# Optimization experiments

Hardware: AMD Instinct MI355X
Metric: run time of the kernel (lower is better)

## Reference

```python
import jax, jax.numpy as jnp
import numpy as np

N = 8192       # n_concepts
D = 128        # embed_dim
L = 2          # n_layers
ALPHA = 0.7
BETA = 0.3
LAM = 0.1      # lambda_decay


def setup_inputs() -> dict:
    key = jax.random.key(0)
    ks = jax.random.split(key, 16)
    adj = jax.random.randint(ks[0], (N, N), 0, 2).astype(jnp.float32)
    s = 0.05
    return {
        "adj": adj,
        "concept_embed": jax.random.normal(ks[1], (N, D), jnp.float32) * s,
        # torch Linear weight is [out,in]; stored here as [in,out] for x @ W
        "gc_w": jax.random.normal(ks[2], (L, D, D), jnp.float32) * s,
        "gc_b": jnp.zeros((L, D), jnp.float32),
        "wq": jax.random.normal(ks[3], (D, D), jnp.float32) * s,
        "bq": jnp.zeros((D,), jnp.float32),
        "wk": jax.random.normal(ks[4], (D, D), jnp.float32) * s,
        "bk": jnp.zeros((D,), jnp.float32),
        "wv": jax.random.normal(ks[5], (D, D), jnp.float32) * s,
        "bv": jnp.zeros((D,), jnp.float32),
        "g1_w": jax.random.normal(ks[6], (4 * D, 2 * D), jnp.float32) * s,
        "g1_b": jnp.zeros((2 * D,), jnp.float32),
        "g2_w": jax.random.normal(ks[7], (2 * D, 4), jnp.float32) * s,
        "g2_b": jnp.zeros((4,), jnp.float32),
        "layer_weights": jnp.ones((L,), jnp.float32) / L,
    }


def _aggregate(E, adj, wq, bq, wk, bk, wv, bv, g1_w, g1_b, g2_w, g2_b):
    nbr = adj != 0                                            # [N,N] neighbor pattern
    nrm = jnp.maximum(jnp.linalg.norm(E, axis=1), 1e-8)       # torch cosine_similarity eps
    sim = (E @ E.T) / (nrm[:, None] * nrm[None, :])           # [N,N] cosine sims
    pos = nbr & (sim >= ALPHA)
    neg = nbr & (sim <= BETA)
    bnd = nbr & (sim > BETA) & (sim < ALPHA)
    posf = pos.astype(E.dtype)
    negf = neg.astype(E.dtype)
    # masked means (zero when region empty, matching torch zeros fallback)
    pos_emb = (posf @ E) / jnp.maximum(posf.sum(1, keepdims=True), 1.0)
    neg_emb = LAM * (negf @ E) / jnp.maximum(negf.sum(1, keepdims=True), 1.0)
    # boundary region: attention of node i over its boundary neighbors
    Q = E @ wq + bq
    K = E @ wk + bk
    V = E @ wv + bv
    s = (Q @ K.T) / np.sqrt(D).astype(np.float32)             # [N,N]
    m = jnp.max(jnp.where(bnd, s, -jnp.inf), axis=1, keepdims=True)
    m = jnp.where(jnp.isfinite(m), m, 0.0)                    # safe max when region empty
    e = jnp.where(bnd, jnp.exp(s - m), 0.0)
    w = e / jnp.maximum(e.sum(1, keepdims=True), 1e-30)       # masked softmax (0 if empty)
    bnd_emb = w @ V
    # gated fusion of [self, pos, bound, neg]
    concat = jnp.concatenate([E, pos_emb, bnd_emb, neg_emb], axis=1)  # [N,4D]
    h = jax.nn.relu(concat @ g1_w + g1_b)
    gate = jax.nn.softmax(h @ g2_w + g2_b, axis=-1)           # [N,4]
    regions = jnp.stack([E, pos_emb, bnd_emb, neg_emb], axis=1)  # [N,4,D]
    fused = jnp.einsum('nr,nrd->nd', gate, regions)
    # nodes with no neighbors keep their own embedding
    return jnp.where(nbr.any(axis=1, keepdims=True), fused, E)


def reference(adj, concept_embed, gc_w, gc_b, wq, bq, wk, bk, wv, bv,
              g1_w, g1_b, g2_w, g2_b, layer_weights):
    cur = concept_embed
    outs = []
    for l in range(L):
        agg = _aggregate(cur, adj, wq, bq, wk, bk, wv, bv, g1_w, g1_b, g2_w, g2_b)
        cur = jax.nn.relu(agg @ gc_w[l] + gc_b[l])
        outs.append(cur)
    lw = jax.nn.softmax(layer_weights)
    return jnp.einsum('l,lnd->nd', lw, jnp.stack(outs))
```

## Files before the change

### kernel.cpp

```cpp
#include <hip/hip_runtime.h>
#include <stdint.h>

#define NN 8192
#define DD 128
#define ALPHA 0.7f
#define BETA 0.3f
#define LAM 0.1f
#define QSCALE 0.08838834764831845f
#define DELTA 3e-5f
#define DELTA_L1 9e-3f
#define FLAGCAP 262144
#define FLAG2CAP 1048576

typedef __attribute__((ext_vector_type(8))) short short8;
typedef __attribute__((ext_vector_type(4))) float f32x4;
typedef unsigned short ush;

__device__ __forceinline__ ush f2bf(float f){
  union { float f; unsigned u; } v; v.f = f;
  return (ush)((v.u + 0x7FFFu + ((v.u >> 16) & 1u)) >> 16);
}
__device__ __forceinline__ float bf2f(ush s){
  union { unsigned u; float f; } v; v.u = ((unsigned)s) << 16; return v.f;
}

__device__ __forceinline__ float qkdot(const ush* __restrict__ Qh,
                                       const ush* __restrict__ Kh,
                                       int i, int j, int lane){
  float q0 = bf2f(Qh[i*DD + lane]),      k0 = bf2f(Kh[j*DD + lane]);
  float q1 = bf2f(Qh[i*DD + 64 + lane]), k1 = bf2f(Kh[j*DD + 64 + lane]);
  float s = q0*k0 + q1*k1;
  #pragma unroll
  for (int m = 32; m; m >>= 1) s += __shfl_xor(s, m, 64);
  return s;
}

__global__ void k_init(const float* __restrict__ adj, unsigned* __restrict__ adjw,
                       const float* __restrict__ wq, const float* __restrict__ wk,
                       const float* __restrict__ wv, const float* __restrict__ g1w,
                       const float* __restrict__ gcw,
                       ush* __restrict__ qkvTh, ush* __restrict__ qkvTl,
                       ush* __restrict__ g1wTh, ush* __restrict__ g1wTl,
                       ush* __restrict__ gcwTh, ush* __restrict__ gcwTl){
  if (blockIdx.x < NN){
    int i = blockIdx.x, wave = threadIdx.x >> 6, lane = threadIdx.x & 63;
    for (int seg = wave; seg < 128; seg += 4){
      int j = seg*64 + lane;
      unsigned long long bm = __ballot(adj[(size_t)i*NN + j] != 0.0f);
      if (lane == 0)  adjw[i*256 + seg*2]     = (unsigned)bm;
      if (lane == 32) adjw[i*256 + seg*2 + 1] = (unsigned)(bm >> 32);
    }
    return;
  }
  int idx = (blockIdx.x - NN)*256 + threadIdx.x;
  const float* src; ush *dh, *dl; int K, Nout, li;
  if      (idx <  16384){ src=wq;        dh=qkvTh;        dl=qkvTl;        K=128; Nout=128; li=idx; }
  else if (idx <  32768){ src=wk;        dh=qkvTh+16384;  dl=qkvTl+16384;  K=128; Nout=128; li=idx-16384; }
  else if (idx <  49152){ src=wv;        dh=qkvTh+32768;  dl=qkvTl+32768;  K=128; Nout=128; li=idx-32768; }
  else if (idx < 180224){ src=g1w;       dh=g1wTh;        dl=g1wTl;        K=512; Nout=256; li=idx-49152; }
  else if (idx < 196608){ src=gcw;       dh=gcwTh;        dl=gcwTl;        K=128; Nout=128; li=idx-180224; }
  else if (idx < 212992){ src=gcw+16384; dh=gcwTh+16384;  dl=gcwTl+16384;  K=128; Nout=128; li=idx-196608; }
  else return;
  int k = li / Nout, n = li - k*Nout;
  float v = src[li];
  ush h = f2bf(v);
  dh[n*K + k] = h;
  dl[n*K + k] = f2bf(v - bf2f(h));
}

__global__ void k_prep(const float* __restrict__ E, double* __restrict__ nrm64,
                       ush* __restrict__ Enh, ush* __restrict__ Enl,
                       ush* __restrict__ EhiT, ush* __restrict__ EloT,
                       const ush* __restrict__ BtH, const ush* __restrict__ BtL,
                       const float* __restrict__ bq, const float* __restrict__ bk,
                       const float* __restrict__ bv,
                       ush* __restrict__ Qh, ush* __restrict__ Kh,
                       ush* __restrict__ VhT, ush* __restrict__ VloT){
  __shared__ float t[64][65];
  __shared__ float sV[128*33];
  int bid = blockIdx.x, tid = threadIdx.x;
  if (bid < 2048){
    int i = bid*4 + (tid >> 6);
    int l = tid & 63;
    float v0 = E[i*DD + l], v1 = E[i*DD + 64 + l];
    double ss = (double)v0*(double)v0 + (double)v1*(double)v1;
    #pragma unroll
    for (int m = 32; m; m >>= 1) ss += __shfl_xor(ss, m, 64);
    double nr = sqrt(ss); if (nr < 1e-8) nr = 1e-8;
    float inv = (float)(1.0 / nr);
    float n0 = v0*inv, n1 = v1*inv;
    ush h0 = f2bf(n0), h1 = f2bf(n1);
    Enh[i*DD + l] = h0;       Enh[i*DD + 64 + l] = h1;
    Enl[i*DD + l] = f2bf(n0 - bf2f(h0));
    Enl[i*DD + 64 + l] = f2bf(n1 - bf2f(h1));
    if (l == 0) nrm64[i] = nr;
  } else if (bid < 2304){
    int lin = bid - 2048;
    int r0 = (lin >> 1) * 64, c0 = (lin & 1) * 64;
    for (int idx = tid; idx < 4096; idx += 256){
      int r = idx >> 6, c = idx & 63;
      t[r][c] = E[(r0 + r)*DD + c0 + c];
    }
    __syncthreads();
    for (int idx = tid; idx < 4096; idx += 256){
      int c = idx >> 6, r = idx & 63;
      float v = t[r][c];
      ush h = f2bf(v);
      EhiT[(size_t)(c0 + c)*NN + r0 + r] = h;
      EloT[(size_t)(c0 + c)*NN + r0 + r] = f2bf(v - bf2f(h));
    }
  } else {
    int lane = tid & 63, wave = tid >> 6;
    int l15 = lane & 15, quad = lane >> 4;
    int rowblk = (bid - 2304) * 32;
    int row16 = rowblk + (wave >> 1)*16;
    int nf0 = (wave & 1)*12;
    f32x4 acc[12];
    #pragma unroll
    for (int i = 0; i < 12; i++){ f32x4 z = {0.f,0.f,0.f,0.f}; acc[i] = z; }
    #pragma unroll
    for (int kk = 0; kk < 4; kk++){
      const float* ap = &E[(row16 + l15)*DD + kk*32 + quad*8];
      short8 ah, al;
      #pragma unroll
      for (int j = 0; j < 8; j++){
        float v = ap[j];
        ush h = f2bf(v);
        ah[j] = (short)h; al[j] = (short)f2bf(v - bf2f(h));
      }
      #pragma unroll
      for (int i = 0; i < 12; i++){
        int bo = ((nf0 + i)*16 + l15)*DD + kk*32 + quad*8;
        short8 bh = *(const short8*)&BtH[bo];
        short8 bl = *(const short8*)&BtL[bo];
        acc[i] = __builtin_amdgcn_mfma_f32_16x16x32_bf16(ah, bh, acc[i], 0, 0, 0);
        acc[i] = __builtin_amdgcn_mfma_f32_16x16x32_bf16(al, bh, acc[i], 0, 0, 0);
        acc[i] = __builtin_amdgcn_mfma_f32_16x16x32_bf16(ah, bl, acc[i], 0, 0, 0);
      }
    }
    #pragma unroll
    for (int i = 0; i < 12; i++){
      int nfg = nf0 + i;
      int grp = nfg >> 3;
      int col = (nfg & 7)*16 + l15;
      float b = (grp == 0) ? bq[col] : (grp == 1) ? bk[col] : bv[col];
      #pragma unroll
      for (int r = 0; r < 4; r++){
        int row = row16 + quad*4 + r;
        float v = acc[i][r] + b;
        if (grp == 0)      Qh[row*DD + col] = f2bf(v * QSCALE);
        else if (grp == 1) Kh[row*DD + col] = f2bf(v);
        else               sV[col*33 + (row - rowblk)] = v;
      }
    }
    __syncthreads();
    int feat = tid >> 1, rh = (tid & 1)*16;
    ush hh[16], ll[16];
    #pragma unroll
    for (int j = 0; j < 16; j++){
      float v = sV[feat*33 + rh + j];
      ush h = f2bf(v);
      hh[j] = h; ll[j] = f2bf(v - bf2f(h));
    }
    size_t go = (size_t)feat*NN + rowblk + rh;
    *(uint4*)&VhT [go]     = *(const uint4*)&hh[0];
    *(uint4*)&VhT [go + 8] = *(const uint4*)&hh[8];
    *(uint4*)&VloT[go]     = *(const uint4*)&ll[0];
    *(uint4*)&VloT[go + 8] = *(const uint4*)&ll[8];
  }
}

__global__ void k_mlp(const float* __restrict__ E, const float* __restrict__ P,
                      const float* __restrict__ B, const float* __restrict__ N,
                      const float* __restrict__ cntP, const float* __restrict__ cntN,
                      const float* __restrict__ denB,
                      const ush* __restrict__ g1Th, const ush* __restrict__ g1Tl,
                      const float* __restrict__ g1b,
                      const float* __restrict__ g2w, const float* __restrict__ g2b,
                      const ush* __restrict__ gcTh, const ush* __restrict__ gcTl,
                      const float* __restrict__ gcb,
                      const float* __restrict__ prevC, const float* __restrict__ lwv,
                      int dofinal, float* __restrict__ out){
  __shared__ float sH[16*260];
  int tid = threadIdx.x, lane = tid & 63, wave = tid >> 6;
  int l15 = lane & 15, quad = lane >> 4;
  int row16 = blockIdx.x*16;
  int row = row16 + l15;
  float cp = cntP[row], cn = cntN[row], dn = denB[row];
  {
    int nf0 = wave*4;
    float rs[4] = {1.f, 1.f/fmaxf(cp,1.f), (dn > 0.5f) ? (1.f/dn) : 0.f, LAM/fmaxf(cn,1.f)};
    const float* bases[4] = {E, P, B, N};
    f32x4 acc[4];
    #pragma unroll
    for (int nf = 0; nf < 4; nf++){ f32x4 z = {0.f,0.f,0.f,0.f}; acc[nf] = z; }
    #pragma unroll
    for (int kk = 0; kk < 16; kk++){
      const float* ap = &bases[kk>>2][row*DD + (kk&3)*32 + quad*8];
      float sc = rs[kk>>2];
      short8 ah, al;
      #pragma unroll
      for (int j = 0; j < 8; j++){
        float v = ap[j] * sc;
        ush h = f2bf(v);
        ah[j] = (short)h; al[j] = (short)f2bf(v - bf2f(h));
      }
      #pragma unroll
      for (int nf = 0; nf < 4; nf++){
        int bo = ((nf0 + nf)*16 + l15)*512 + kk*32 + quad*8;
        short8 bh = *(const short8*)&g1Th[bo];
        short8 bl = *(const short8*)&g1Tl[bo];
        acc[nf] = __builtin_amdgcn_mfma_f32_16x16x32_bf16(ah, bh, acc[nf], 0, 0, 0);
        acc[nf] = __builtin_amdgcn_mfma_f32_16x16x32_bf16(al, bh, acc[nf], 0, 0, 0);
        acc[nf] = __builtin_amdgcn_mfma_f32_16x16x32_bf16(ah, bl, acc[nf], 0, 0, 0);
      }
    }
    #pragma unroll
    for (int nf = 0; nf < 4; nf++){
      int col = (nf0 + nf)*16 + l15;
      float b = g1b[col];
      #pragma unroll
      for (int r = 0; r < 4; r++)
        sH[(quad*4 + r)*260 + col] = fmaxf(acc[nf][r] + b, 0.f);
    }
  }
  __syncthreads();
  {
    int nf0 = wave*2;
    float l0=0,l1=0,l2=0,l3=0;
    #pragma unroll
    for (int i = 0; i < 16; i++){
      float4 hv = *(const float4*)&sH[l15*260 + quad*64 + i*4];
      float hvv[4] = {hv.x, hv.y, hv.z, hv.w};
      #pragma unroll
      for (int j = 0; j < 4; j++){
        float4 w4 = *(const float4*)&g2w[(quad*64 + i*4 + j)*4];
        l0 = fmaf(hvv[j], w4.x, l0); l1 = fmaf(hvv[j], w4.y, l1);
        l2 = fmaf(hvv[j], w4.z, l2); l3 = fmaf(hvv[j], w4.w, l3);
      }
    }
    l0 += __shfl_xor(l0,16,64); l0 += __shfl_xor(l0,32,64);
    l1 += __shfl_xor(l1,16,64); l1 += __shfl_xor(l1,32,64);
    l2 += __shfl_xor(l2,16,64); l2 += __shfl_xor(l2,32,64);
    l3 += __shfl_xor(l3,16,64); l3 += __shfl_xor(l3,32,64);
    l0 += g2b[0]; l1 += g2b[1]; l2 += g2b[2]; l3 += g2b[3];
    float mx = fmaxf(fmaxf(l0,l1), fmaxf(l2,l3));
    float e0 = __expf(l0-mx), e1 = __expf(l1-mx), e2 = __expf(l2-mx), e3 = __expf(l3-mx);
    float inv = 1.f/(e0+e1+e2+e3);
    float g0 = e0*inv, g1v = e1*inv, g2v = e2*inv, g3 = e3*inv;
    bool any = (cp + cn > 0.5f) || (dn > 0.5f);
    float pscl = g1v/fmaxf(cp,1.f);
    float bscl = (dn > 0.5f) ? (g2v/dn) : 0.f;
    float nscl = LAM*g3/fmaxf(cn,1.f);
    f32x4 acc[2];
    #pragma unroll
    for (int nf = 0; nf < 2; nf++){ f32x4 z = {0.f,0.f,0.f,0.f}; acc[nf] = z; }
    #pragma unroll
    for (int kk = 0; kk < 4; kk++){
      int koff = row*DD + kk*32 + quad*8;
      short8 ah, al;
      #pragma unroll
      for (int j = 0; j < 8; j++){
        float ev = E[koff + j];
        float v = any ? (g0*ev + pscl*P[koff+j] + bscl*B[koff+j] + nscl*N[koff+j]) : ev;
        ush h = f2bf(v);
        ah[j] = (short)h; al[j] = (short)f2bf(v - bf2f(h));
      }
      #pragma unroll
      for (int nf = 0; nf < 2; nf++){
        int bo = ((nf0 + nf)*16 + l15)*DD + kk*32 + quad*8;
        short8 bh = *(const short8*)&gcTh[bo];
        short8 bl = *(const short8*)&gcTl[bo];
        acc[nf] = __builtin_amdgcn_mfma_f32_16x16x32_bf16(ah, bh, acc[nf], 0, 0, 0);
        acc[nf] = __builtin_amdgcn_mfma_f32_16x16x32_bf16(al, bh, acc[nf], 0, 0, 0);
        acc[nf] = __builtin_amdgcn_mfma_f32_16x16x32_bf16(ah, bl, acc[nf], 0, 0, 0);
      }
    }
    float we0 = 0.5f, we1 = 0.5f;
    if (dofinal){
      float a0 = lwv[0], a1 = lwv[1];
      float mw = fmaxf(a0, a1);
      float x0 = __expf(a0-mw), x1 = __expf(a1-mw);
      float iv = 1.f/(x0+x1);
      we0 = x0*iv; we1 = x1*iv;
    }
    #pragma unroll
    for (int nf = 0; nf < 2; nf++){
      int col = (nf0 + nf)*16 + l15;
      float b = gcb[col];
      #pragma unroll
      for (int r = 0; r < 4; r++){
        int rr = row16 + quad*4 + r;
        float val = fmaxf(acc[nf][r] + b, 0.f);
        if (dofinal) val = we0*prevC[rr*DD + col] + we1*val;
        out[rr*DD + col] = val;
      }
    }
  }
}

#define BM 64
#define BN 32
#define CSPLIT 4
#define CCHUNK (NN/CSPLIT)
#define NTILES (CCHUNK/BN)
#define RSTRIDE 136
#define FSTRIDE 80
#define MSTRIDE 80

template<int DENSEB>
__launch_bounds__(256, 2)
__global__ void k_fused(const unsigned* __restrict__ adjw,
    const ush* __restrict__ Enh, const ush* __restrict__ Enl,
    const ush* __restrict__ Qh,  const ush* __restrict__ Kh,
    const ush* __restrict__ EhiT, const ush* __restrict__ EloT,
    const ush* __restrict__ VhT,  const ush* __restrict__ VloT,
    float* __restrict__ Nsum, float* __restrict__ Bsum,
    float* __restrict__ cntN, float* __restrict__ denB,
    int* __restrict__ flagCnt, float4* __restrict__ flags,
    int* __restrict__ flag2Cnt, float4* __restrict__ flags2)
{
  __shared__ __attribute__((aligned(16))) ush sEnh[32*RSTRIDE];
  __shared__ __attribute__((aligned(16))) ush sEnl[DENSEB ? 32*RSTRIDE : 16];
  __shared__ __attribute__((aligned(16))) ush sKh [DENSEB ? 32*RSTRIDE : 16];
  __shared__ __attribute__((aligned(16))) ush sE2 [128*FSTRIDE];
  __shared__ __attribute__((aligned(16))) ush sV2 [DENSEB ? 128*FSTRIDE : 16];
  __shared__ __attribute__((aligned(16))) ush sM  [4][16*MSTRIDE];

  const float del = DENSEB ? DELTA : DELTA_L1;
  int tid = threadIdx.x, lane = tid & 63, wave = tid >> 6;
  int l15 = lane & 15, quad = lane >> 4;
  int rowblk = blockIdx.x >> 2, split = blockIdx.x & 3;
  int row0 = rowblk * BM + wave * 16;
  int col0 = split * CCHUNK;

  short8 bEnh[4], bEnl[4], bQ[4];
  #pragma unroll
  for (int kf = 0; kf < 4; kf++){
    int go = (row0 + l15)*DD + kf*32 + quad*8;
    bEnh[kf] = *(const short8*)&Enh[go];
    if (DENSEB){
      bEnl[kf] = *(const short8*)&Enl[go];
      bQ[kf] = *(const short8*)&Qh[go];
    }
  }

  f32x4 accN[8], accB[DENSEB ? 8 : 1];
  #pragma unroll
  for (int nf = 0; nf < 8; nf++){ f32x4 z = {0.f,0.f,0.f,0.f}; accN[nf]=z; }
  if (DENSEB){
    #pragma unroll
    for (int nf = 0; nf < 8; nf++){ f32x4 z = {0.f,0.f,0.f,0.f}; accB[nf]=z; }
  }
  float cnL = 0.f, dbL = 0.f;

  int f0 = tid >> 2,        n0 = (tid & 3)*8;
  int f1 = (tid+256) >> 2,  n1 = ((tid+256) & 3)*8;
  uint4 pEh0, pEh1, pVh0, pVh1;
  {
    size_t g0 = (size_t)f0*NN + col0 + n0, g1 = (size_t)f1*NN + col0 + n1;
    pEh0 = *(const uint4*)&EhiT[g0]; pEh1 = *(const uint4*)&EhiT[g1];
    if (DENSEB){
      pVh0 = *(const uint4*)&VhT [g0]; pVh1 = *(const uint4*)&VhT [g1];
    }
  }
  int rr0 = tid >> 4,       ro0 = (tid & 15)*8;
  int rr1 = (tid+256) >> 4, ro1 = ((tid+256) & 15)*8;

  for (int t = 0; t < NTILES; t++){
    int c0 = col0 + t*BN;
    __syncthreads();
    *(uint4*)&sE2[f0*FSTRIDE + n0] = pEh0;  *(uint4*)&sE2[f1*FSTRIDE + n1] = pEh1;
    if (DENSEB){
      *(uint4*)&sV2[f0*FSTRIDE + n0] = pVh0;  *(uint4*)&sV2[f1*FSTRIDE + n1] = pVh1;
    }
    {
      uint4 a0 = *(const uint4*)&Enh[(c0 + rr0)*DD + ro0];
      uint4 a1 = *(const uint4*)&Enh[(c0 + rr1)*DD + ro1];
      *(uint4*)&sEnh[rr0*RSTRIDE + ro0] = a0;  *(uint4*)&sEnh[rr1*RSTRIDE + ro1] = a1;
      if (DENSEB){
        uint4 b0 = *(const uint4*)&Enl[(c0 + rr0)*DD + ro0];
        uint4 b1 = *(const uint4*)&Enl[(c0 + rr1)*DD + ro1];
        uint4 k0 = *(const uint4*)&Kh [(c0 + rr0)*DD + ro0];
        uint4 k1 = *(const uint4*)&Kh [(c0 + rr1)*DD + ro1];
        *(uint4*)&sEnl[rr0*RSTRIDE + ro0] = b0;  *(uint4*)&sEnl[rr1*RSTRIDE + ro1] = b1;
        *(uint4*)&sKh [rr0*RSTRIDE + ro0] = k0;  *(uint4*)&sKh [rr1*RSTRIDE + ro1] = k1;
      }
    }
    __syncthreads();
    if (t + 1 < NTILES){
      int c1 = c0 + BN;
      size_t g0 = (size_t)f0*NN + c1 + n0, g1 = (size_t)f1*NN + c1 + n1;
      pEh0 = *(const uint4*)&EhiT[g0]; pEh1 = *(const uint4*)&EhiT[g1];
      if (DENSEB){
        pVh0 = *(const uint4*)&VhT [g0]; pVh1 = *(const uint4*)&VhT [g1];
      }
    }
    unsigned aw = adjw[(row0 + l15)*256 + (c0 >> 5)];

    f32x4 simT[2], svT[2];
    { f32x4 z = {0.f,0.f,0.f,0.f}; simT[0]=z; simT[1]=z; svT[0]=z; svT[1]=z; }
    #pragma unroll
    for (int f = 0; f < 2; f++){
      #pragma unroll
      for (int kf = 0; kf < 4; kf++){
        int la = (f*16 + l15)*RSTRIDE + kf*32 + quad*8;
        short8 ch = *(const short8*)&sEnh[la];
        simT[f] = __builtin_amdgcn_mfma_f32_16x16x32_bf16(ch, bEnh[kf], simT[f],0,0,0);
        if (DENSEB){
          short8 cl = *(const short8*)&sEnl[la];
          short8 ck = *(const short8*)&sKh [la];
          simT[f] = __builtin_amdgcn_mfma_f32_16x16x32_bf16(cl, bEnh[kf], simT[f],0,0,0);
          simT[f] = __builtin_amdgcn_mfma_f32_16x16x32_bf16(ch, bEnl[kf], simT[f],0,0,0);
          svT [f] = __builtin_amdgcn_mfma_f32_16x16x32_bf16(ck, bQ  [kf], svT [f],0,0,0);
        }
      }
    }
    ushort4 ehv[2];
    unsigned flagb = 0, spb = 0;
    #pragma unroll
    for (int f = 0; f < 2; f++){
      ush vn2[4], veh[4];
      #pragma unroll
      for (int r = 0; r < 4; r++){
        int cbit = f*16 + quad*4 + r;
        bool nbr = (aw >> cbit) & 1u;
        float c = simT[f][r];
        bool pos = nbr && (c >= ALPHA);
        bool neg = nbr && (c <= BETA);
        bool bnd = nbr && !pos && !neg;
        vn2[r] = neg ? (ush)0x3F80 : (ush)0;
        cnL += neg ? 1.f : 0.f;
        if (DENSEB){
          float e = bnd ? __expf(svT[f][r]) : 0.f;
          veh[r] = f2bf(e);
          dbL += e;
        }
        if (nbr && (fabsf(c - ALPHA) < del || fabsf(c - BETA) < del))
          flagb |= 1u << (f*4 + r);
        if (pos || (!DENSEB && bnd))
          spb |= 1u << (f*4 + r);
      }
      int mb = l15*MSTRIDE + f*16 + quad*4;
      *(ushort4*)&sM[wave][mb] = make_ushort4(vn2[0],vn2[1],vn2[2],vn2[3]);
      if (DENSEB)
        ehv[f] = make_ushort4(veh[0],veh[1],veh[2],veh[3]);
    }
    if (__ballot((flagb | spb) != 0)){
      #pragma unroll
      for (int f = 0; f < 2; f++){
        #pragma unroll
        for (int r = 0; r < 4; r++){
          int bit = f*4 + r;
          bool fl = (flagb >> bit) & 1u;
          unsigned long long bm = __ballot(fl);
          if (bm){
            int leader = __ffsll((long long)bm) - 1;
            int base = 0;
            if (lane == leader) base = atomicAdd(flagCnt, __popcll(bm));
            base = __shfl(base, leader, 64);
            if (fl){
              int id = base + __popcll(bm & ((1ull << lane) - 1ull));
              if (id < FLAGCAP){
                float4 rec;
                rec.x = __int_as_float(row0 + l15);
                rec.y = __int_as_float(c0 + f*16 + quad*4 + r);
                rec.z = simT[f][r];
                rec.w = DENSEB ? svT[f][r] : 0.f;
                flags[id] = rec;
              }
            }
          }
          bool f2 = (spb >> bit) & 1u;
          unsigned long long bm2 = __ballot(f2);
          if (bm2){
            int leader = __ffsll((long long)bm2) - 1;
            int base = 0;
            if (lane == leader) base = atomicAdd(flag2Cnt, __popcll(bm2));
            base = __shfl(base, leader, 64);
            if (f2){
              int id = base + __popcll(bm2 & ((1ull << lane) - 1ull));
              if (id < FLAG2CAP){
                float c = simT[f][r];
                int j = c0 + f*16 + quad*4 + r;
                int cls = (c >= ALPHA) ? 0 : 1;
                float4 rec;
                rec.x = __int_as_float(row0 + l15);
                rec.y = __int_as_float(j | (cls << 16));
                rec.z = c;
                rec.w = DENSEB ? svT[f][r] : 0.f;
                flags2[id] = rec;
              }
            }
          }
        }
      }
    }
    {
      short8 mNeg = *(const short8*)&sM[wave][l15*MSTRIDE + quad*8];
      #pragma unroll
      for (int nf = 0; nf < 8; nf++){
        int so = (nf*16 + l15)*FSTRIDE + quad*8;
        short8 eth = *(const short8*)&sE2[so];
        accN[nf] = __builtin_amdgcn_mfma_f32_16x16x32_bf16(mNeg, eth, accN[nf],0,0,0);
      }
    }
    if (DENSEB){
      int mb0 = l15*MSTRIDE + quad*4;
      *(ushort4*)&sM[wave][mb0]      = ehv[0];
      *(ushort4*)&sM[wave][mb0 + 16] = ehv[1];
      short8 mEh = *(const short8*)&sM[wave][l15*MSTRIDE + quad*8];
      #pragma unroll
      for (int nf = 0; nf < 8; nf++){
        int so = (nf*16 + l15)*FSTRIDE + quad*8;
        short8 vth = *(const short8*)&sV2[so];
        accB[nf] = __builtin_amdgcn_mfma_f32_16x16x32_bf16(mEh, vth, accB[nf],0,0,0);
      }
    }
  }
  #pragma unroll
  for (int nf = 0; nf < 8; nf++){
    int col = nf*16 + l15;
    #pragma unroll
    for (int r = 0; r < 4; r++){
      int row = row0 + quad*4 + r;
      atomicAdd(&Nsum[row*DD + col], accN[nf][r]);
      if (DENSEB) atomicAdd(&Bsum[row*DD + col], accB[nf][r]);
    }
  }
  cnL += __shfl_xor(cnL, 16, 64); cnL += __shfl_xor(cnL, 32, 64);
  if (DENSEB){ dbL += __shfl_xor(dbL, 16, 64); dbL += __shfl_xor(dbL, 32, 64); }
  if (quad == 0){
    atomicAdd(&cntN[row0 + l15], cnL);
    if (DENSEB) atomicAdd(&denB[row0 + l15], dbL);
  }
}

__global__ void k_fix(const float* __restrict__ E, const double* __restrict__ nrm64,
    const ush* __restrict__ EhiT, const ush* __restrict__ EloT,
    const ush* __restrict__ VhT,  const ush* __restrict__ VloT,
    const ush* __restrict__ Qh,   const ush* __restrict__ Kh, int dotmode,
    const int* __restrict__ flag2Cnt, const float4* __restrict__ flags2,
    const int* __restrict__ flagCnt,  const float4* __restrict__ flags,
    float* __restrict__ Psum, float* __restrict__ Nsum, float* __restrict__ Bsum,
    float* __restrict__ cntP, float* __restrict__ cntN, float* __restrict__ denB)
{
  int lane = threadIdx.x & 63;
  if (blockIdx.x < 256){
    int cnt = *flag2Cnt; if (cnt > FLAG2CAP) cnt = FLAG2CAP;
    int gw = (blockIdx.x * blockDim.x + threadIdx.x) >> 6;
    int nw = (256 * blockDim.x) >> 6;
    for (int idx = gw; idx < cnt; idx += nw){
      float4 rec = flags2[idx];
      int i = __float_as_int(rec.x);
      int jraw = __float_as_int(rec.y);
      int j = jraw & 0xFFFF, cls = jraw >> 16;
      if (cls == 0){
        #pragma unroll
        for (int h = 0; h < 2; h++){
          int d = lane + h*64;
          float ev = bf2f(EhiT[(size_t)d*NN + j]) + bf2f(EloT[(size_t)d*NN + j]);
          atomicAdd(&Psum[i*DD + d], ev);
        }
        if (lane == 0) atomicAdd(&cntP[i], 1.f);
      } else {
        float s = dotmode ? qkdot(Qh, Kh, i, j, lane) : rec.w;
        float e = __expf(s);
        float ehf = bf2f(f2bf(e));
        float elf = bf2f(f2bf(e - ehf));
        #pragma unroll
        for (int h = 0; h < 2; h++){
          int d = lane + h*64;
          float vh = bf2f(VhT [(size_t)d*NN + j]);
          float bv = ehf*vh;
          if (dotmode) bv += elf*vh + ehf*bf2f(VloT[(size_t)d*NN + j]);
          atomicAdd(&Bsum[i*DD + d], bv);
        }
        if (lane == 0) atomicAdd(&denB[i], e);
      }
    }
  } else {
    int cnt = *flagCnt; if (cnt > FLAGCAP) cnt = FLAGCAP;
    int gw = ((blockIdx.x - 256) * blockDim.x + threadIdx.x) >> 6;
    int nw = (512 * blockDim.x) >> 6;
    for (int idx = gw; idx < cnt; idx += nw){
      float4 rec = flags[idx];
      int i = __float_as_int(rec.x), j = __float_as_int(rec.y);
      float c = rec.z;
      float ei0 = E[i*DD + lane], ei1 = E[i*DD + 64 + lane];
      float ej0 = E[j*DD + lane], ej1 = E[j*DD + 64 + lane];
      double d = (double)ei0*(double)ej0 + (double)ei1*(double)ej1;
      #pragma unroll
      for (int m = 32; m; m >>= 1) d += __shfl_xor(d, m, 64);
      double se = d / (nrm64[i]*nrm64[j]);
      int ce = (se >= (double)ALPHA) ? 0 : ((se <= (double)BETA) ? 1 : 2);
      int cc = (c >= ALPHA) ? 0 : ((c <= BETA) ? 1 : 2);
      if (ce == cc) continue;
      float s = dotmode ? qkdot(Qh, Kh, i, j, lane) : rec.w;
      float e = __expf(s);
      float ehf = bf2f(f2bf(e));
      float elf = bf2f(f2bf(e - ehf));
      #pragma unroll
      for (int h = 0; h < 2; h++){
        int dd2 = lane + h*64;
        float evh = bf2f(EhiT[(size_t)dd2*NN + j]);
        float evp = evh + bf2f(EloT[(size_t)dd2*NN + j]);
        float vh = bf2f(VhT[(size_t)dd2*NN + j]);
        float bv = ehf*vh;
        if (dotmode) bv += elf*vh + ehf*bf2f(VloT[(size_t)dd2*NN + j]);
        float subv = (cc==0) ? -evp : (cc==1) ? -evh : -bv;
        float* subA = (cc==0) ? Psum : (cc==1) ? Nsum : Bsum;
        atomicAdd(&subA[i*DD + dd2], subv);
        float addv = (ce==0) ? evp : (ce==1) ? evh : bv;
        float* addA = (ce==0) ? Psum : (ce==1) ? Nsum : Bsum;
        atomicAdd(&addA[i*DD + dd2], addv);
      }
      if (lane == 0){
        float* subC = (cc==0) ? cntP : (cc==1) ? cntN : denB;
        atomicAdd(&subC[i], (cc==2) ? -e : -1.f);
        float* addC = (ce==0) ? cntP : (ce==1) ? cntN : denB;
        atomicAdd(&addC[i], (ce==2) ?  e :  1.f);
      }
    }
  }
}

extern "C" void kernel_launch(void* const* d_in, const int* in_sizes, int n_in,
                              void* d_out, int out_size, void* d_ws, size_t ws_size,
                              hipStream_t stream){
  const float* adj   = (const float*)d_in[0];
  const float* embed = (const float*)d_in[1];
  const float* gc_w  = (const float*)d_in[2];
  const float* gc_b  = (const float*)d_in[3];
  const float* wq = (const float*)d_in[4];
  const float* bq = (const float*)d_in[5];
  const float* wk = (const float*)d_in[6];
  const float* bk = (const float*)d_in[7];
  const float* wv = (const float*)d_in[8];
  const float* bv = (const float*)d_in[9];
  const float* g1w = (const float*)d_in[10];
  const float* g1b = (const float*)d_in[11];
  const float* g2w = (const float*)d_in[12];
  const float* g2b = (const float*)d_in[13];
  const float* lw  = (const float*)d_in[14];
  float* out = (float*)d_out;

  char* p = (char*)d_ws;
  auto alloc = [&](size_t bytes)->void*{ void* r = (void*)p; p += (bytes + 255) & ~(size_t)255; return r; };
  ush* qkvTh = (ush*)alloc(384*128*2);  ush* qkvTl = (ush*)alloc(384*128*2);
  ush* g1wTh = (ush*)alloc(512*256*2);  ush* g1wTl = (ush*)alloc(512*256*2);
  ush* gcwTh = (ush*)alloc(2*128*128*2); ush* gcwTl = (ush*)alloc(2*128*128*2);
  unsigned* adjw = (unsigned*)alloc((size_t)NN*256*4);
  double* nrm64 = (double*)alloc(NN*8);
  ush* Enh  = (ush*)alloc((size_t)NN*DD*2);
  ush* Enl  = (ush*)alloc((size_t)NN*DD*2);
  ush* EhiT = (ush*)alloc((size_t)NN*DD*2);
  ush* EloT = (ush*)alloc((size_t)NN*DD*2);
  ush* Qh   = (ush*)alloc((size_t)NN*DD*2);
  ush* Khb  = (ush*)alloc((size_t)NN*DD*2);
  ush* VhT  = (ush*)alloc((size_t)NN*DD*2);
  ush* VloT = (ush*)alloc((size_t)NN*DD*2);
  char* zbase = p;
  float* Psum = (float*)alloc((size_t)NN*DD*4);
  float* Nsum = (float*)alloc((size_t)NN*DD*4);
  float* Bsum = (float*)alloc((size_t)NN*DD*4);
  float* cntP = (float*)alloc(NN*4);
  float* cntN = (float*)alloc(NN*4);
  float* denB = (float*)alloc(NN*4);
  int*   flagCnt  = (int*)alloc(256);
  int*   flag2Cnt = (int*)alloc(256);
  size_t zbytes = (size_t)(p - zbase);
  float4* flags  = (float4*)alloc((size_t)FLAGCAP*16);
  float4* flags2 = (float4*)alloc((size_t)FLAG2CAP*16);
  float* cur0 = (float*)alloc((size_t)NN*DD*4);

  k_init<<<NN + 832, 256, 0, stream>>>(adj, adjw, wq, wk, wv, g1w, gc_w,
      qkvTh, qkvTl, g1wTh, g1wTl, gcwTh, gcwTl);

  const float* Ecur = embed;
  for (int l = 0; l < 2; l++){
    k_prep<<<2560, 256, 0, stream>>>(Ecur, nrm64, Enh, Enl, EhiT, EloT,
        qkvTh, qkvTl, bq, bk, bv, Qh, Khb, VhT, VloT);
    hipMemsetAsync(zbase, 0, zbytes, stream);
    if (l == 0)
      k_fused<0><<<(NN/BM)*CSPLIT, 256, 0, stream>>>(adjw, Enh, Enl, Qh, Khb,
          EhiT, EloT, VhT, VloT, Nsum, Bsum, cntN, denB,
          flagCnt, flags, flag2Cnt, flags2);
    else
      k_fused<1><<<(NN/BM)*CSPLIT, 256, 0, stream>>>(adjw, Enh, Enl, Qh, Khb,
          EhiT, EloT, VhT, VloT, Nsum, Bsum, cntN, denB,
          flagCnt, flags, flag2Cnt, flags2);
    k_fix<<<768, 256, 0, stream>>>(Ecur, nrm64, EhiT, EloT, VhT, VloT,
        Qh, Khb, (l == 0) ? 1 : 0, flag2Cnt, flags2, flagCnt, flags,
        Psum, Nsum, Bsum, cntP, cntN, denB);
    k_mlp<<<512, 256, 0, stream>>>(Ecur, Psum, Bsum, Nsum, cntP, cntN, denB,
        g1wTh, g1wTl, g1b, g2w, g2b,
        gcwTh + l*128*128, gcwTl + l*128*128, gc_b + l*128,
        cur0, lw, l, (l == 0) ? cur0 : out);
    Ecur = (l == 0) ? cur0 : out;
  }
}
```

Baseline: 1.045 ms.

## Double column split in fused kernel and replace atomics with partial-sum reduction

Raises the column split from 4 to 8 so the fused kernel launches twice as many blocks. It shrinks the shared-memory strides to match the smaller chunk and raises occupancy hints to 3 blocks per CU. Per-split partial sums are written to separate buffers with plain stores instead of float atomics, and a new reduce kernel sums them before the fix stage. This trades atomic contention for roughly 64 MB of extra partial-buffer traffic and one more kernel launch per layer.

```diff
diff --git a/kernel.cpp b/kernel.cpp
--- a/kernel.cpp
+++ b/kernel.cpp
@@ -167,6 +167,44 @@
     *(uint4*)&VhT [go + 8] = *(const uint4*)&hh[8];
     *(uint4*)&VloT[go]     = *(const uint4*)&ll[0];
     *(uint4*)&VloT[go + 8] = *(const uint4*)&ll[8];
+  }
+}
+
+__global__ void k_reduce(const float4* __restrict__ NsumP, const float4* __restrict__ BsumP,
+                         const float* __restrict__ cntNP, const float* __restrict__ denBP,
+                         float4* __restrict__ Nsum, float4* __restrict__ Bsum,
+                         float* __restrict__ cntN, float* __restrict__ denB, int doB){
+  const int NE4 = NN*DD/4;
+  int idx = blockIdx.x*256 + threadIdx.x;
+  if (idx < NE4){
+    float4 a = NsumP[idx];
+    #pragma unroll
+    for (int s = 1; s < 8; s++){
+      float4 u = NsumP[(size_t)s*NE4 + idx];
+      a.x += u.x; a.y += u.y; a.z += u.z; a.w += u.w;
+    }
+    Nsum[idx] = a;
+    if (doB){
+      float4 b = BsumP[idx];
+      #pragma unroll
+      for (int s = 1; s < 8; s++){
+        float4 u = BsumP[(size_t)s*NE4 + idx];
+        b.x += u.x; b.y += u.y; b.z += u.z; b.w += u.w;
+      }
+      Bsum[idx] = b;
+    }
+  } else if (idx < NE4 + NN){
+    int r = idx - NE4;
+    float c = 0.f;
+    #pragma unroll
+    for (int s = 0; s < 8; s++) c += cntNP[s*NN + r];
+    cntN[r] = c;
+    if (doB){
+      float d2 = 0.f;
+      #pragma unroll
+      for (int s = 0; s < 8; s++) d2 += denBP[s*NN + r];
+      denB[r] = d2;
+    }
   }
 }
 
@@ -301,22 +339,22 @@
 
 #define BM 64
 #define BN 32
-#define CSPLIT 4
+#define CSPLIT 8
 #define CCHUNK (NN/CSPLIT)
 #define NTILES (CCHUNK/BN)
 #define RSTRIDE 136
-#define FSTRIDE 80
-#define MSTRIDE 80
+#define FSTRIDE 40
+#define MSTRIDE 40
 
 template<int DENSEB>
-__launch_bounds__(256, 2)
+__launch_bounds__(256, 3)
 __global__ void k_fused(const unsigned* __restrict__ adjw,
     const ush* __restrict__ Enh, const ush* __restrict__ Enl,
     const ush* __restrict__ Qh,  const ush* __restrict__ Kh,
     const ush* __restrict__ EhiT, const ush* __restrict__ EloT,
     const ush* __restrict__ VhT,  const ush* __restrict__ VloT,
-    float* __restrict__ Nsum, float* __restrict__ Bsum,
-    float* __restrict__ cntN, float* __restrict__ denB,
+    float* __restrict__ NsumP, float* __restrict__ BsumP,
+    float* __restrict__ cntNP, float* __restrict__ denBP,
     int* __restrict__ flagCnt, float4* __restrict__ flags,
     int* __restrict__ flag2Cnt, float4* __restrict__ flags2)
 {
@@ -330,7 +368,7 @@
   const float del = DENSEB ? DELTA : DELTA_L1;
   int tid = threadIdx.x, lane = tid & 63, wave = tid >> 6;
   int l15 = lane & 15, quad = lane >> 4;
-  int rowblk = blockIdx.x >> 2, split = blockIdx.x & 3;
+  int rowblk = blockIdx.x >> 3, split = blockIdx.x & 7;
   int row0 = rowblk * BM + wave * 16;
   int col0 = split * CCHUNK;
 
@@ -518,21 +556,23 @@
       }
     }
   }
+  float* Np = NsumP + (size_t)split*(NN*DD);
+  float* Bp = BsumP + (size_t)split*(NN*DD);
   #pragma unroll
   for (int nf = 0; nf < 8; nf++){
     int col = nf*16 + l15;
     #pragma unroll
     for (int r = 0; r < 4; r++){
       int row = row0 + quad*4 + r;
-      atomicAdd(&Nsum[row*DD + col], accN[nf][r]);
-      if (DENSEB) atomicAdd(&Bsum[row*DD + col], accB[nf][r]);
+      Np[row*DD + col] = accN[nf][r];
+      if (DENSEB) Bp[row*DD + col] = accB[nf][r];
     }
   }
   cnL += __shfl_xor(cnL, 16, 64); cnL += __shfl_xor(cnL, 32, 64);
   if (DENSEB){ dbL += __shfl_xor(dbL, 16, 64); dbL += __shfl_xor(dbL, 32, 64); }
   if (quad == 0){
-    atomicAdd(&cntN[row0 + l15], cnL);
-    if (DENSEB) atomicAdd(&denB[row0 + l15], dbL);
+    cntNP[split*NN + row0 + l15] = cnL;
+    if (DENSEB) denBP[split*NN + row0 + l15] = dbL;
   }
 }
 
@@ -660,12 +700,16 @@
   ush* Khb  = (ush*)alloc((size_t)NN*DD*2);
   ush* VhT  = (ush*)alloc((size_t)NN*DD*2);
   ush* VloT = (ush*)alloc((size_t)NN*DD*2);
+  float* NsumP = (float*)alloc((size_t)8*NN*DD*4);
+  float* BsumP = (float*)alloc((size_t)8*NN*DD*4);
+  float* cntNP = (float*)alloc((size_t)8*NN*4);
+  float* denBP = (float*)alloc((size_t)8*NN*4);
+  float* Nsum = (float*)alloc((size_t)NN*DD*4);
+  float* cntN = (float*)alloc(NN*4);
   char* zbase = p;
   float* Psum = (float*)alloc((size_t)NN*DD*4);
-  float* Nsum = (float*)alloc((size_t)NN*DD*4);
   float* Bsum = (float*)alloc((size_t)NN*DD*4);
   float* cntP = (float*)alloc(NN*4);
-  float* cntN = (float*)alloc(NN*4);
   float* denB = (float*)alloc(NN*4);
   int*   flagCnt  = (int*)alloc(256);
   int*   flag2Cnt = (int*)alloc(256);
@@ -684,12 +728,15 @@
     hipMemsetAsync(zbase, 0, zbytes, stream);
     if (l == 0)
       k_fused<0><<<(NN/BM)*CSPLIT, 256, 0, stream>>>(adjw, Enh, Enl, Qh, Khb,
-          EhiT, EloT, VhT, VloT, Nsum, Bsum, cntN, denB,
+          EhiT, EloT, VhT, VloT, NsumP, BsumP, cntNP, denBP,
           flagCnt, flags, flag2Cnt, flags2);
     else
       k_fused<1><<<(NN/BM)*CSPLIT, 256, 0, stream>>>(adjw, Enh, Enl, Qh, Khb,
-          EhiT, EloT, VhT, VloT, Nsum, Bsum, cntN, denB,
+          EhiT, EloT, VhT, VloT, NsumP, BsumP, cntNP, denBP,
           flagCnt, flags, flag2Cnt, flags2);
+    k_reduce<<<(NN*DD/4 + NN + 255)/256, 256, 0, stream>>>(
+        (const float4*)NsumP, (const float4*)BsumP, cntNP, denBP,
+        (float4*)Nsum, (float4*)Bsum, cntN, denB, l);
     k_fix<<<768, 256, 0, stream>>>(Ecur, nrm64, EhiT, EloT, VhT, VloT,
         Qh, Khb, (l == 0) ? 1 : 0, flag2Cnt, flags2, flagCnt, flags,
         Psum, Nsum, Bsum, cntP, cntN, denB);
```

Result: slower. 1.423 ms (+36.2%).
